# Kernel optimization log

Measured on AMD Instinct MI355X. Metric: run time of the kernel, lower is better.

The kernel has to match this reference:

```python
import jax, jax.numpy as jnp
import numpy as np

EPS = 1e-8
LN_EPS = 1e-5
TOPK = 8

B, N, D = 8, 2048, 512


def setup_inputs() -> dict:
    key = jax.random.key(0)
    ks = jax.random.split(key, 4)
    feats = jax.random.normal(ks[0], (B, N, D), dtype=jnp.float32)
    mask = jnp.ones((B, N), dtype=bool)
    # per-layer GCN weights (no bias) and LayerNorm params, plus output LN
    W1 = jax.random.normal(ks[1], (D, D), dtype=jnp.float32) / np.sqrt(D)
    W2 = jax.random.normal(ks[2], (D, D), dtype=jnp.float32) / np.sqrt(D)
    ln1_g = jnp.ones((D,), jnp.float32); ln1_b = jnp.zeros((D,), jnp.float32)
    ln2_g = jnp.ones((D,), jnp.float32); ln2_b = jnp.zeros((D,), jnp.float32)
    out_g = jnp.ones((D,), jnp.float32); out_b = jnp.zeros((D,), jnp.float32)
    return {"feats": feats, "mask": mask, "W1": W1, "ln1_g": ln1_g, "ln1_b": ln1_b,
            "W2": W2, "ln2_g": ln2_g, "ln2_b": ln2_b, "out_g": out_g, "out_b": out_b}


def _layer_norm(x, g, b):
    mu = jnp.mean(x, axis=-1, keepdims=True)
    var = jnp.mean(jnp.square(x - mu), axis=-1, keepdims=True)
    return (x - mu) * jax.lax.rsqrt(var + LN_EPS) * g + b


def build_similarity_graph(feats, mask):
    b, n, _ = feats.shape
    mask_f = mask.astype(feats.dtype)                       # [B,N]
    valid_pair = mask[:, None, :] & mask[:, :, None]        # [B,N,N]
    vp_f = valid_pair.astype(feats.dtype)
    # cosine similarity mapped to [0,1]
    fn = feats / jnp.clip(jnp.linalg.norm(feats, axis=-1, keepdims=True), EPS)
    sim = (jnp.einsum('bnd,bmd->bnm', fn, fn) + 1.0) * 0.5
    sim = sim * vp_f
    eye = jnp.eye(n, dtype=bool)
    sim_wo_self = jnp.where(eye[None], 0.0, sim)
    # top-k neighbors per node (invalid pairs pushed to -1)
    k = min(TOPK, n - 1)
    candidate = jnp.where(valid_pair, sim_wo_self, -1.0)
    values, indices = jax.lax.top_k(candidate, k)           # [B,N,k]
    bi = jnp.arange(b)[:, None, None]
    ri = jnp.arange(n)[None, :, None]
    knn_mask = jnp.zeros((b, n, n), dtype=bool).at[bi, ri, indices].set(values > 0)
    adj = sim_wo_self * knn_mask.astype(feats.dtype)
    # symmetrize, add valid self-loops, re-mask
    adj = 0.5 * (adj + jnp.swapaxes(adj, 1, 2))
    adj = adj + jnp.eye(n, dtype=feats.dtype)[None] * (mask_f[:, :, None] * mask_f[:, None, :])
    adj = adj * vp_f
    # symmetric degree normalization
    deg_inv_sqrt = jnp.clip(adj.sum(-1), EPS) ** -0.5       # [B,N]
    adj_norm = adj * deg_inv_sqrt[:, :, None] * deg_inv_sqrt[:, None, :]
    return adj_norm * vp_f


def _gcn_layer(x, adj_norm, W, g, b, mask_f):
    out = jnp.einsum('bnm,bmd->bnd', adj_norm, x @ W) + x   # residual (Identity proj)
    out = jax.nn.relu(_layer_norm(out, g, b))
    return out * mask_f[..., None]


def reference(feats, mask, W1, ln1_g, ln1_b, W2, ln2_g, ln2_b, out_g, out_b):
    mask_f = mask.astype(feats.dtype)
    x = feats * mask_f[..., None]                           # input_proj = Identity, then mask
    adj_norm = build_similarity_graph(feats, mask)
    x = _gcn_layer(x, adj_norm, W1, ln1_g, ln1_b, mask_f)
    x = _gcn_layer(x, adj_norm, W2, ln2_g, ln2_b, mask_f)
    x = _layer_norm(x, out_g, out_b)
    return x * mask_f[..., None]
```

## Files before the change

### kernel.cpp

```cpp
#include <hip/hip_runtime.h>
#include <cstdint>


constexpr int Bb   = 8;
constexpr int Nn   = 2048;
constexpr int Dd   = 512;
constexpr int BN   = Bb * Nn;
constexpr int KTOP = 8;
constexpr int CAP  = 56;
constexpr int NSLICE = 4;

typedef __attribute__((ext_vector_type(8))) __bf16 bf16x8;
typedef __attribute__((ext_vector_type(4))) __bf16 bf16x4;
typedef __attribute__((ext_vector_type(4))) float  f32x4;

__device__ __forceinline__ void gload16(const void* g, void* l) {
  __builtin_amdgcn_global_load_lds((const __attribute__((address_space(1))) unsigned int*)g,
                                   (__attribute__((address_space(3))) unsigned int*)l,
                                   16, 0, 0);
}
__device__ __forceinline__ void barrier_raw() {
  asm volatile("" ::: "memory");
  __builtin_amdgcn_s_barrier();
  asm volatile("" ::: "memory");
}

__global__ __launch_bounds__(256) void rownorm_kernel(const float* __restrict__ feats,
                                                      float* __restrict__ rinv) {
  const int row  = blockIdx.x * 4 + (threadIdx.x >> 6);
  const int lane = threadIdx.x & 63;
  const float* p = feats + (size_t)row * Dd + lane * 8;
  float4 a = *(const float4*)p;
  float4 b = *(const float4*)(p + 4);
  float s = a.x*a.x + a.y*a.y + a.z*a.z + a.w*a.w
          + b.x*b.x + b.y*b.y + b.z*b.z + b.w*b.w;
#pragma unroll
  for (int o = 32; o; o >>= 1) s += __shfl_down(s, o);
  if (lane == 0) rinv[row] = 1.0f / fmaxf(sqrtf(s), 1e-8f);
}

__global__ __launch_bounds__(256) void split_kernel(const float* __restrict__ feats,
                                                    const float* __restrict__ rinv,
                                                    __bf16* __restrict__ Hk,
                                                    __bf16* __restrict__ Lk,
                                                    __bf16* __restrict__ Xk) {
  __shared__ float tile[64][65];
  __shared__ float rsh[64];
  const int r0 = blockIdx.x * 64;
  const int bz = r0 >> 11;
  const int n0 = r0 & 2047;
  const int t  = threadIdx.x;
  if (t < 64) rsh[t] = rinv[r0 + t];

  for (int kt = 0; kt < 8; ++kt) {
    __syncthreads();
#pragma unroll
    for (int p = 0; p < 4; ++p) {
      const int row = p * 16 + (t >> 4), ch = t & 15;
      float4 v = *(const float4*)(feats + (size_t)(r0 + row) * Dd + kt * 64 + ch * 4);
      tile[row][ch * 4 + 0] = v.x; tile[row][ch * 4 + 1] = v.y;
      tile[row][ch * 4 + 2] = v.z; tile[row][ch * 4 + 3] = v.w;
    }
    __syncthreads();
#pragma unroll
    for (int h = 0; h < 2; ++h) {
      const int c = h * 256 + t;
      const int k8l = c >> 6, row = c & 63;
      const float s = rsh[row];
      bf16x8 hv, lv, xv;
#pragma unroll
      for (int e = 0; e < 8; ++e) {
        const float x = tile[row][k8l * 8 + e];
        xv[e] = (__bf16)x;
        const float nm = x * s;
        const __bf16 hh = (__bf16)nm;
        hv[e] = hh;
        lv[e] = (__bf16)(nm - (float)hh);
      }
      const size_t kk = (size_t)(kt * 8 + k8l);
      *(bf16x8*)(Hk + ((size_t)(bz * 64) + kk) * (Nn * 8) + (n0 + row) * 8) = hv;
      *(bf16x8*)(Lk + ((size_t)(bz * 64) + kk) * (Nn * 8) + (n0 + row) * 8) = lv;
      *(bf16x8*)(Xk + kk * ((size_t)BN * 8) + (size_t)(r0 + row) * 8) = xv;
    }
  }
}

__global__ __launch_bounds__(256) void wcast_t(const float* __restrict__ W,
                                               __bf16* __restrict__ Wk) {
  __shared__ float t[32][33];
  const int bx = blockIdx.x * 32, by = blockIdx.y * 32;
  const int lx = threadIdx.x & 31, ly = threadIdx.x >> 5;
#pragma unroll
  for (int r = 0; r < 32; r += 8)
    t[ly + r][lx] = W[(size_t)(by + ly + r) * Dd + bx + lx];
  __syncthreads();
  if (threadIdx.x < 128) {
    const int k8l = threadIdx.x >> 5, nl = threadIdx.x & 31;
    bf16x8 v;
#pragma unroll
    for (int e = 0; e < 8; ++e) v[e] = (__bf16)t[k8l * 8 + e][nl];
    *(bf16x8*)(Wk + ((size_t)((by >> 3) + k8l) * Dd + bx + nl) * 8) = v;
  }
}

__device__ __forceinline__ void ins8(float (&tv)[8], int (&ti)[8], float v, int idx) {
#pragma unroll
  for (int q = 0; q < 8; ++q) {
    bool sw = v > tv[q];
    float a = sw ? tv[q] : v;
    int   c = sw ? ti[q] : idx;
    tv[q] = sw ? v   : tv[q];
    ti[q] = sw ? idx : ti[q];
    v = a; idx = c;
  }
}
__device__ __forceinline__ void ins8t(float (&tv)[8], int (&ti)[8], float v, int idx) {
#pragma unroll
  for (int q = 0; q < 8; ++q) {
    bool sw = (v > tv[q]) || (v == tv[q] && idx < ti[q]);
    float a = sw ? tv[q] : v;
    int   c = sw ? ti[q] : idx;
    tv[q] = sw ? v   : tv[q];
    ti[q] = sw ? idx : ti[q];
    v = a; idx = c;
  }
}

__global__ __launch_bounds__(256, 2) void sim_mfma_topk(const __bf16* __restrict__ Hk,
                                                        const __bf16* __restrict__ Lk,
                                                        float* __restrict__ pv,
                                                        int* __restrict__ pi) {
  __shared__ __align__(16) char smem[65536];

  const int f     = blockIdx.x;
  const int bz    = f & 7;
  const int rr    = f >> 3;
  const int r0    = (rr & 15) * 128;
  const int slice = rr >> 4;

  const int tid    = threadIdx.x;
  const int lane   = tid & 63;
  const int lane15 = tid & 15;
  const int kgrp   = (tid >> 4) & 3;
  const int wv     = tid >> 6;
  const int wrow0  = wv * 32;
  const int bN     = bz * Nn;

  const __bf16* Hb = Hk + (size_t)(bz * 64) * (Nn * 8);
  const __bf16* Lb = Lk + (size_t)(bz * 64) * (Nn * 8);

  float t8v[2][8]; int t8i[2][8];
#pragma unroll
  for (int rs = 0; rs < 2; ++rs)
#pragma unroll
    for (int q = 0; q < 8; ++q) { t8v[rs][q] = -1.0f; t8i[rs][q] = 0; }

  auto stage = [&](int t, int buf) {
    const int ct = t >> 4, k80 = (t & 15) << 2;
    const int rbase = (wv < 2) ? r0 : slice * 512 + ct * 128;
    const __bf16* base = ((wv & 1) == 0) ? Hb : Lb;
    char* ldsb = smem + buf * 32768 + wv * 8192;
#pragma unroll
    for (int i = 0; i < 8; ++i) {
      const int kg = i >> 1, rb = (i & 1) << 6;
      gload16(base + ((size_t)(k80 + kg) * Nn + rbase + rb + lane) * 8,
              ldsb + kg * 2048 + rb * 16);
    }
  };

  f32x4 acc[2][8];
  const f32x4 z = {0.f, 0.f, 0.f, 0.f};

  stage(0, 0);
  for (int t = 0; t < 64; ++t) {
    const int cur = t & 1;
    if ((t & 15) == 0) {
#pragma unroll
      for (int i = 0; i < 2; ++i)
#pragma unroll
        for (int j = 0; j < 8; ++j) acc[i][j] = z;
    }
    if (t + 1 < 64) {
      stage(t + 1, cur ^ 1);
      asm volatile("s_waitcnt vmcnt(8)" ::: "memory");
    } else {
      asm volatile("s_waitcnt vmcnt(0)" ::: "memory");
    }
    barrier_raw();

    const char* sb = smem + cur * 32768;
    const int a0o = kgrp * 2048 + (wrow0 + lane15) * 16;
    bf16x8 ah0 = *(const bf16x8*)(sb + a0o);
    bf16x8 ah1 = *(const bf16x8*)(sb + a0o + 256);
    bf16x8 al0 = *(const bf16x8*)(sb + 8192 + a0o);
    bf16x8 al1 = *(const bf16x8*)(sb + 8192 + a0o + 256);
#pragma unroll
    for (int cs = 0; cs < 8; ++cs) {
      const int bo = kgrp * 2048 + (cs * 16 + lane15) * 16;
      bf16x8 bh = *(const bf16x8*)(sb + 16384 + bo);
      bf16x8 bl = *(const bf16x8*)(sb + 24576 + bo);
      acc[0][cs] = __builtin_amdgcn_mfma_f32_16x16x32_bf16(bh, ah0, acc[0][cs], 0, 0, 0);
      acc[0][cs] = __builtin_amdgcn_mfma_f32_16x16x32_bf16(bl, ah0, acc[0][cs], 0, 0, 0);
      acc[0][cs] = __builtin_amdgcn_mfma_f32_16x16x32_bf16(bh, al0, acc[0][cs], 0, 0, 0);
      acc[1][cs] = __builtin_amdgcn_mfma_f32_16x16x32_bf16(bh, ah1, acc[1][cs], 0, 0, 0);
      acc[1][cs] = __builtin_amdgcn_mfma_f32_16x16x32_bf16(bl, ah1, acc[1][cs], 0, 0, 0);
      acc[1][cs] = __builtin_amdgcn_mfma_f32_16x16x32_bf16(bh, al1, acc[1][cs], 0, 0, 0);
    }
    barrier_raw();

    if ((t & 15) == 15) {
      const int ct = t >> 4;
      const int ctile0 = slice * 512 + ct * 128;
#pragma unroll
      for (int rs = 0; rs < 2; ++rs) {
        const int rowg = r0 + wrow0 + rs * 16 + lane15;
#pragma unroll
        for (int cs = 0; cs < 8; ++cs)
#pragma unroll
          for (int e = 0; e < 4; ++e) {
            const int col = ctile0 + cs * 16 + kgrp * 4 + e;
            const float v = (acc[rs][cs][e] + 1.0f) * 0.5f;
            if (col != rowg && v > t8v[rs][7]) ins8(t8v[rs], t8i[rs], v, col);
          }
      }
    }
  }

#pragma unroll
  for (int rs = 0; rs < 2; ++rs) {
#pragma unroll
    for (int m = 16; m <= 32; m <<= 1) {
      float ov[8]; int oi[8];
#pragma unroll
      for (int q = 0; q < 8; ++q) {
        ov[q] = __shfl_xor(t8v[rs][q], m);
        oi[q] = __shfl_xor(t8i[rs][q], m);
      }
#pragma unroll
      for (int q = 0; q < 8; ++q)
        if (ov[q] > t8v[rs][7] || (ov[q] == t8v[rs][7] && oi[q] < t8i[rs][7]))
          ins8t(t8v[rs], t8i[rs], ov[q], oi[q]);
    }
  }

  if (lane < 16) {
#pragma unroll
    for (int rs = 0; rs < 2; ++rs) {
      const int prow = bN + r0 + wrow0 + rs * 16 + lane15;
#pragma unroll
      for (int q = 0; q < 8; ++q) {
        pv[(prow * NSLICE + slice) * 8 + q] = t8v[rs][q];
        pi[(prow * NSLICE + slice) * 8 + q] = bN + t8i[rs][q];
      }
    }
  }
}

__global__ __launch_bounds__(256) void merge_edges(const float* __restrict__ pv,
                                                   const int* __restrict__ pi,
                                                   int* __restrict__ ecnt,
                                                   int* __restrict__ eidx,
                                                   float* __restrict__ ew) {
  const int row = blockIdx.x * 256 + threadIdx.x;
  if (row >= BN) return;
  float tv[8]; int ti[8];
#pragma unroll
  for (int q = 0; q < 8; ++q) { tv[q] = -1.0f; ti[q] = 0; }
  for (int s = 0; s < NSLICE; ++s)
#pragma unroll
    for (int q = 0; q < 8; ++q) {
      const float v = pv[(row * NSLICE + s) * 8 + q];
      if (v > tv[7]) ins8(tv, ti, v, pi[(row * NSLICE + s) * 8 + q]);
    }
#pragma unroll
  for (int t = 0; t < KTOP; ++t) {
    if (tv[t] > 0.0f) {
      const int j = ti[t];
      const float w = 0.5f * tv[t];
      int p = atomicAdd(&ecnt[row], 1);
      if (p < CAP) { eidx[row * CAP + p] = j; ew[row * CAP + p] = w; }
      int q2 = atomicAdd(&ecnt[j], 1);
      if (q2 < CAP) { eidx[j * CAP + q2] = row; ew[j * CAP + q2] = w; }
    }
  }
}

__global__ __launch_bounds__(256) void deg_kernel(const int* __restrict__ ecnt,
                                                  const float* __restrict__ ew,
                                                  float* __restrict__ dis) {
  const int r = blockIdx.x * 256 + threadIdx.x;
  if (r >= BN) return;
  const int cnt = min(ecnt[r], CAP);
  float d = 1.0f;
  for (int e = 0; e < cnt; ++e) d += ew[r * CAP + e];
  dis[r] = rsqrtf(fmaxf(d, 1e-8f));
}

__global__ __launch_bounds__(256, 2) void gemm_mfma(const __bf16* __restrict__ Xk,
                                                    const __bf16* __restrict__ Wk,
                                                    __bf16* __restrict__ Yb) {
  __shared__ __align__(16) char smem[32768];
  const int tid    = threadIdx.x;
  const int lane   = tid & 63;
  const int lane15 = tid & 15;
  const int kgrp   = (tid >> 4) & 3;
  const int wv     = tid >> 6;
  const int m0 = blockIdx.x * 128, n0 = blockIdx.y * 128;

  auto stage = [&](int t, int buf) {
    const int k80 = t << 2;
#pragma unroll
    for (int i = 0; i < 4; ++i) {
      const int c = (wv << 2) + i;
      const int kg = (c & 7) >> 1, rb = (c & 1) << 6;
      const __bf16* g = (c >> 3)
          ? Wk + ((size_t)(k80 + kg) * Dd + n0 + rb + lane) * 8
          : Xk + ((size_t)(k80 + kg) * BN + m0 + rb + lane) * 8;
      gload16(g, smem + buf * 16384 + ((c >> 3) << 13) + kg * 2048 + rb * 16);
    }
  };

  f32x4 acc[2][8];
  const f32x4 z = {0.f, 0.f, 0.f, 0.f};
#pragma unroll
  for (int i = 0; i < 2; ++i)
#pragma unroll
    for (int j = 0; j < 8; ++j) acc[i][j] = z;

  stage(0, 0);
  for (int t = 0; t < 16; ++t) {
    const int cur = t & 1;
    if (t + 1 < 16) {
      stage(t + 1, cur ^ 1);
      asm volatile("s_waitcnt vmcnt(4)" ::: "memory");
    } else {
      asm volatile("s_waitcnt vmcnt(0)" ::: "memory");
    }
    barrier_raw();

    const char* sb = smem + cur * 16384;
    const int a0o = kgrp * 2048 + (wv * 32 + lane15) * 16;
    bf16x8 a0 = *(const bf16x8*)(sb + a0o);
    bf16x8 a1 = *(const bf16x8*)(sb + a0o + 256);
#pragma unroll
    for (int cs = 0; cs < 8; ++cs) {
      bf16x8 b = *(const bf16x8*)(sb + 8192 + kgrp * 2048 + (cs * 16 + lane15) * 16);
      acc[0][cs] = __builtin_amdgcn_mfma_f32_16x16x32_bf16(b, a0, acc[0][cs], 0, 0, 0);
      acc[1][cs] = __builtin_amdgcn_mfma_f32_16x16x32_bf16(b, a1, acc[1][cs], 0, 0, 0);
    }
    barrier_raw();
  }
#pragma unroll
  for (int rs = 0; rs < 2; ++rs) {
    const int row = m0 + wv * 32 + rs * 16 + lane15;
#pragma unroll
    for (int cs = 0; cs < 8; ++cs) {
      bf16x4 o;
#pragma unroll
      for (int e = 0; e < 4; ++e) o[e] = (__bf16)acc[rs][cs][e];
      *(bf16x4*)(Yb + (size_t)row * Dd + n0 + cs * 16 + kgrp * 4) = o;
    }
  }
}

__device__ __forceinline__ void breduce2_128(float& s, float& q, float* red) {
#pragma unroll
  for (int o = 32; o; o >>= 1) { s += __shfl_down(s, o); q += __shfl_down(q, o); }
  __syncthreads();
  if ((threadIdx.x & 63) == 0) {
    red[(threadIdx.x >> 6) * 2]     = s;
    red[(threadIdx.x >> 6) * 2 + 1] = q;
  }
  __syncthreads();
  s = red[0] + red[2];
  q = red[1] + red[3];
}

template <bool FINAL>
__global__ __launch_bounds__(128) void agg_ln_kernel(const __bf16* __restrict__ yb,
                                                     const float* __restrict__ xres_f,
                                                     const __bf16* __restrict__ xres_k,
                                                     const int* __restrict__ ecnt,
                                                     const int* __restrict__ eidx,
                                                     const float* __restrict__ ew,
                                                     const float* __restrict__ dis,
                                                     const float* __restrict__ g1,
                                                     const float* __restrict__ b1v,
                                                     const float* __restrict__ g2,
                                                     const float* __restrict__ b2v,
                                                     float* __restrict__ outf,
                                                     __bf16* __restrict__ outk) {
  __shared__ float red[4];
  const int row = (blockIdx.x & 7) * Nn + (blockIdx.x >> 3);
  const int tid = threadIdx.x;
  const int d0 = tid * 4;
  const float di = dis[row];

  bf16x4 yv = *(const bf16x4*)(yb + (size_t)row * Dd + d0);
  float a[4];
#pragma unroll
  for (int e2 = 0; e2 < 4; ++e2) a[e2] = di * di * (float)yv[e2];
  const int cnt = min(ecnt[row], CAP);
  for (int e = 0; e < cnt; ++e) {
    const int j = eidx[row * CAP + e];
    const float c = ew[row * CAP + e] * di * dis[j];
    bf16x4 v = *(const bf16x4*)(yb + (size_t)j * Dd + d0);
#pragma unroll
    for (int e2 = 0; e2 < 4; ++e2) a[e2] += c * (float)v[e2];
  }
  if (FINAL) {
    bf16x4 u = *(const bf16x4*)(xres_k + ((size_t)(tid >> 1) * BN + row) * 8 + (tid & 1) * 4);
#pragma unroll
    for (int e2 = 0; e2 < 4; ++e2) a[e2] += (float)u[e2];
  } else {
    float4 xv = *(const float4*)(xres_f + (size_t)row * Dd + d0);
    a[0] += xv.x; a[1] += xv.y; a[2] += xv.z; a[3] += xv.w;
  }

  float s = a[0] + a[1] + a[2] + a[3];
  float qq = a[0]*a[0] + a[1]*a[1] + a[2]*a[2] + a[3]*a[3];
  breduce2_128(s, qq, red);
  const float mu = s * (1.0f / Dd);
  const float var = qq * (1.0f / Dd) - mu * mu;
  const float rs = rsqrtf(var + 1e-5f);
  float4 g = *(const float4*)(g1 + d0);
  float4 bb = *(const float4*)(b1v + d0);
  float tv[4];
  tv[0] = fmaxf((a[0] - mu) * rs * g.x + bb.x, 0.0f);
  tv[1] = fmaxf((a[1] - mu) * rs * g.y + bb.y, 0.0f);
  tv[2] = fmaxf((a[2] - mu) * rs * g.z + bb.z, 0.0f);
  tv[3] = fmaxf((a[3] - mu) * rs * g.w + bb.w, 0.0f);

  if (FINAL) {
    float s2 = tv[0] + tv[1] + tv[2] + tv[3];
    float q2 = tv[0]*tv[0] + tv[1]*tv[1] + tv[2]*tv[2] + tv[3]*tv[3];
    breduce2_128(s2, q2, red);
    const float mu2 = s2 * (1.0f / Dd);
    const float var2 = q2 * (1.0f / Dd) - mu2 * mu2;
    const float rs2 = rsqrtf(var2 + 1e-5f);
    float4 g2v = *(const float4*)(g2 + d0);
    float4 b2 = *(const float4*)(b2v + d0);
    float4 o;
    o.x = (tv[0] - mu2) * rs2 * g2v.x + b2.x;
    o.y = (tv[1] - mu2) * rs2 * g2v.y + b2.y;
    o.z = (tv[2] - mu2) * rs2 * g2v.z + b2.z;
    o.w = (tv[3] - mu2) * rs2 * g2v.w + b2.w;
    *(float4*)(outf + (size_t)row * Dd + d0) = o;
  } else {
    bf16x4 ov;
#pragma unroll
    for (int e2 = 0; e2 < 4; ++e2) ov[e2] = (__bf16)tv[e2];
    *(bf16x4*)(outk + ((size_t)(tid >> 1) * BN + row) * 8 + (tid & 1) * 4) = ov;
  }
}

extern "C" void kernel_launch(void* const* d_in, const int* in_sizes, int n_in,
                              void* d_out, int out_size, void* d_ws, size_t ws_size,
                              hipStream_t stream) {
  const float* feats = (const float*)d_in[0];
  const float* W1    = (const float*)d_in[2];
  const float* ln1_g = (const float*)d_in[3];
  const float* ln1_b = (const float*)d_in[4];
  const float* W2    = (const float*)d_in[5];
  const float* ln2_g = (const float*)d_in[6];
  const float* ln2_b = (const float*)d_in[7];
  const float* out_g = (const float*)d_in[8];
  const float* out_b = (const float*)d_in[9];
  float* out = (float*)d_out;

  char* w = (char*)d_ws;
  float* rinv = (float*)w; w += (size_t)BN * 4;
  float* topv = (float*)w; w += (size_t)BN * KTOP * 4;
  int*   topi = (int*)w;   w += (size_t)BN * KTOP * 4;
  int*   ecnt = (int*)w;   w += (size_t)BN * 4;
  int*   eidx = (int*)w;   w += (size_t)BN * CAP * 4;
  float* ew   = (float*)w; w += (size_t)BN * CAP * 4;
  float* dis  = (float*)w; w += (size_t)BN * 4;
  __bf16* Wk1 = (__bf16*)w; w += (size_t)Dd * Dd * 2;
  __bf16* Wk2 = (__bf16*)w; w += (size_t)Dd * Dd * 2;
  float* ybuf = (float*)w; w += (size_t)BN * Dd * 4;
  __bf16* Xk  = (__bf16*)w; w += (size_t)BN * Dd * 2;
  __bf16* h1k = (__bf16*)w; w += (size_t)BN * Dd * 2;
  __bf16* Hk = (__bf16*)ybuf;
  __bf16* Lk = Hk + (size_t)BN * Dd;
  __bf16* Yb = (__bf16*)ybuf;
  float* pv  = (float*)h1k;
  int*   pi  = (int*)((char*)h1k + (size_t)BN * NSLICE * 8 * 4);
  (void)topv; (void)topi;

  hipMemsetAsync(ecnt, 0, (size_t)BN * 4, stream);

  rownorm_kernel<<<BN / 4, 256, 0, stream>>>(feats, rinv);
  split_kernel<<<BN / 64, 256, 0, stream>>>(feats, rinv, Hk, Lk, Xk);
  wcast_t<<<dim3(16, 16), 256, 0, stream>>>(W1, Wk1);
  wcast_t<<<dim3(16, 16), 256, 0, stream>>>(W2, Wk2);

  sim_mfma_topk<<<512, 256, 0, stream>>>(Hk, Lk, pv, pi);
  merge_edges<<<BN / 256, 256, 0, stream>>>(pv, pi, ecnt, eidx, ew);
  deg_kernel<<<BN / 256, 256, 0, stream>>>(ecnt, ew, dis);

  gemm_mfma<<<dim3(BN / 128, Dd / 128), 256, 0, stream>>>(Xk, Wk1, Yb);
  agg_ln_kernel<false><<<BN, 128, 0, stream>>>(Yb, feats, nullptr, ecnt, eidx, ew, dis,
                                               ln1_g, ln1_b, nullptr, nullptr,
                                               nullptr, h1k);
  gemm_mfma<<<dim3(BN / 128, Dd / 128), 256, 0, stream>>>(h1k, Wk2, Yb);
  agg_ln_kernel<true><<<BN, 128, 0, stream>>>(Yb, nullptr, h1k, ecnt, eidx, ew, dis,
                                              ln2_g, ln2_b, out_g, out_b,
                                              out, nullptr);
}
```

Baseline: 315.2 us.

## Replace split-bf16 similarity with single bf16 pass plus fp32 top-k refinement

The similarity GEMM drops the hi/lo bf16 split (three MFMAs per tile) and uses a single bf16 product, halving LDS staging and allowing more slices and blocks. Each slice keeps its approximate top-8. A new refine kernel picks the 12 best candidates per row from the 64 and recomputes their exact fp32 cosine from feats before choosing the final top-8. The row-norm kernel is folded into split_kernel. In exchange, a true neighbour that bf16 rounding pushes out of a slice's top-8 or outside the 12 refined candidates would be missed.

```diff
diff --git a/kernel.cpp b/kernel.cpp
--- a/kernel.cpp
+++ b/kernel.cpp
@@ -8,7 +8,7 @@
 constexpr int BN   = Bb * Nn;
 constexpr int KTOP = 8;
 constexpr int CAP  = 56;
-constexpr int NSLICE = 4;
+constexpr int NSLICE = 8;
 
 typedef __attribute__((ext_vector_type(8))) __bf16 bf16x8;
 typedef __attribute__((ext_vector_type(4))) __bf16 bf16x4;
@@ -25,24 +25,9 @@
   asm volatile("" ::: "memory");
 }
 
-__global__ __launch_bounds__(256) void rownorm_kernel(const float* __restrict__ feats,
-                                                      float* __restrict__ rinv) {
-  const int row  = blockIdx.x * 4 + (threadIdx.x >> 6);
-  const int lane = threadIdx.x & 63;
-  const float* p = feats + (size_t)row * Dd + lane * 8;
-  float4 a = *(const float4*)p;
-  float4 b = *(const float4*)(p + 4);
-  float s = a.x*a.x + a.y*a.y + a.z*a.z + a.w*a.w
-          + b.x*b.x + b.y*b.y + b.z*b.z + b.w*b.w;
-#pragma unroll
-  for (int o = 32; o; o >>= 1) s += __shfl_down(s, o);
-  if (lane == 0) rinv[row] = 1.0f / fmaxf(sqrtf(s), 1e-8f);
-}
-
 __global__ __launch_bounds__(256) void split_kernel(const float* __restrict__ feats,
-                                                    const float* __restrict__ rinv,
+                                                    float* __restrict__ rinv,
                                                     __bf16* __restrict__ Hk,
-                                                    __bf16* __restrict__ Lk,
                                                     __bf16* __restrict__ Xk) {
   __shared__ float tile[64][65];
   __shared__ float rsh[64];
@@ -50,7 +35,23 @@
   const int bz = r0 >> 11;
   const int n0 = r0 & 2047;
   const int t  = threadIdx.x;
-  if (t < 64) rsh[t] = rinv[r0 + t];
+  const int wv = t >> 6, lane = t & 63;
+
+  for (int i = 0; i < 16; ++i) {
+    const int row = wv * 16 + i;
+    const float* p = feats + (size_t)(r0 + row) * Dd + lane * 8;
+    float4 a = *(const float4*)p;
+    float4 b = *(const float4*)(p + 4);
+    float s = a.x*a.x + a.y*a.y + a.z*a.z + a.w*a.w
+            + b.x*b.x + b.y*b.y + b.z*b.z + b.w*b.w;
+#pragma unroll
+    for (int o = 32; o; o >>= 1) s += __shfl_down(s, o);
+    if (lane == 0) {
+      const float ri = 1.0f / fmaxf(sqrtf(s), 1e-8f);
+      rsh[row] = ri;
+      rinv[r0 + row] = ri;
+    }
+  }
 
   for (int kt = 0; kt < 8; ++kt) {
     __syncthreads();
@@ -67,19 +68,15 @@
       const int c = h * 256 + t;
       const int k8l = c >> 6, row = c & 63;
       const float s = rsh[row];
-      bf16x8 hv, lv, xv;
+      bf16x8 hv, xv;
 #pragma unroll
       for (int e = 0; e < 8; ++e) {
         const float x = tile[row][k8l * 8 + e];
         xv[e] = (__bf16)x;
-        const float nm = x * s;
-        const __bf16 hh = (__bf16)nm;
-        hv[e] = hh;
-        lv[e] = (__bf16)(nm - (float)hh);
+        hv[e] = (__bf16)(x * s);
       }
       const size_t kk = (size_t)(kt * 8 + k8l);
       *(bf16x8*)(Hk + ((size_t)(bz * 64) + kk) * (Nn * 8) + (n0 + row) * 8) = hv;
-      *(bf16x8*)(Lk + ((size_t)(bz * 64) + kk) * (Nn * 8) + (n0 + row) * 8) = lv;
       *(bf16x8*)(Xk + kk * ((size_t)BN * 8) + (size_t)(r0 + row) * 8) = xv;
     }
   }
@@ -126,11 +123,10 @@
   }
 }
 
-__global__ __launch_bounds__(256, 2) void sim_mfma_topk(const __bf16* __restrict__ Hk,
-                                                        const __bf16* __restrict__ Lk,
-                                                        float* __restrict__ pv,
-                                                        int* __restrict__ pi) {
-  __shared__ __align__(16) char smem[65536];
+__global__ __launch_bounds__(256, 3) void sim_hh_topk(const __bf16* __restrict__ Hk,
+                                                      float* __restrict__ pv,
+                                                      int* __restrict__ pi) {
+  __shared__ __align__(16) char smem[32768];
 
   const int f     = blockIdx.x;
   const int bz    = f & 7;
@@ -147,7 +143,6 @@
   const int bN     = bz * Nn;
 
   const __bf16* Hb = Hk + (size_t)(bz * 64) * (Nn * 8);
-  const __bf16* Lb = Lk + (size_t)(bz * 64) * (Nn * 8);
 
   float t8v[2][8]; int t8i[2][8];
 #pragma unroll
@@ -157,14 +152,16 @@
 
   auto stage = [&](int t, int buf) {
     const int ct = t >> 4, k80 = (t & 15) << 2;
-    const int rbase = (wv < 2) ? r0 : slice * 512 + ct * 128;
-    const __bf16* base = ((wv & 1) == 0) ? Hb : Lb;
-    char* ldsb = smem + buf * 32768 + wv * 8192;
-#pragma unroll
-    for (int i = 0; i < 8; ++i) {
-      const int kg = i >> 1, rb = (i & 1) << 6;
-      gload16(base + ((size_t)(k80 + kg) * Nn + rbase + rb + lane) * 8,
-              ldsb + kg * 2048 + rb * 16);
+    const int c0 = slice * 256 + ct * 128;
+#pragma unroll
+    for (int i = 0; i < 4; ++i) {
+      const int c = (wv << 2) + i;
+      const bool isB = c >= 8;
+      const int cc = isB ? c - 8 : c;
+      const int kg = cc >> 1, rb = cc & 1;
+      const int rbase = (isB ? c0 : r0) + rb * 64 + lane;
+      gload16(Hb + ((size_t)(k80 + kg) * Nn + rbase) * 8,
+              smem + buf * 16384 + (isB ? 8192 : 0) + kg * 2048 + (rb * 64 + lane) * 16);
     }
   };
 
@@ -172,7 +169,7 @@
   const f32x4 z = {0.f, 0.f, 0.f, 0.f};
 
   stage(0, 0);
-  for (int t = 0; t < 64; ++t) {
+  for (int t = 0; t < 32; ++t) {
     const int cur = t & 1;
     if ((t & 15) == 0) {
 #pragma unroll
@@ -180,37 +177,29 @@
 #pragma unroll
         for (int j = 0; j < 8; ++j) acc[i][j] = z;
     }
-    if (t + 1 < 64) {
+    if (t + 1 < 32) {
       stage(t + 1, cur ^ 1);
-      asm volatile("s_waitcnt vmcnt(8)" ::: "memory");
+      asm volatile("s_waitcnt vmcnt(4)" ::: "memory");
     } else {
       asm volatile("s_waitcnt vmcnt(0)" ::: "memory");
     }
     barrier_raw();
 
-    const char* sb = smem + cur * 32768;
+    const char* sb = smem + cur * 16384;
     const int a0o = kgrp * 2048 + (wrow0 + lane15) * 16;
     bf16x8 ah0 = *(const bf16x8*)(sb + a0o);
     bf16x8 ah1 = *(const bf16x8*)(sb + a0o + 256);
-    bf16x8 al0 = *(const bf16x8*)(sb + 8192 + a0o);
-    bf16x8 al1 = *(const bf16x8*)(sb + 8192 + a0o + 256);
 #pragma unroll
     for (int cs = 0; cs < 8; ++cs) {
-      const int bo = kgrp * 2048 + (cs * 16 + lane15) * 16;
-      bf16x8 bh = *(const bf16x8*)(sb + 16384 + bo);
-      bf16x8 bl = *(const bf16x8*)(sb + 24576 + bo);
+      bf16x8 bh = *(const bf16x8*)(sb + 8192 + kgrp * 2048 + (cs * 16 + lane15) * 16);
       acc[0][cs] = __builtin_amdgcn_mfma_f32_16x16x32_bf16(bh, ah0, acc[0][cs], 0, 0, 0);
-      acc[0][cs] = __builtin_amdgcn_mfma_f32_16x16x32_bf16(bl, ah0, acc[0][cs], 0, 0, 0);
-      acc[0][cs] = __builtin_amdgcn_mfma_f32_16x16x32_bf16(bh, al0, acc[0][cs], 0, 0, 0);
       acc[1][cs] = __builtin_amdgcn_mfma_f32_16x16x32_bf16(bh, ah1, acc[1][cs], 0, 0, 0);
-      acc[1][cs] = __builtin_amdgcn_mfma_f32_16x16x32_bf16(bl, ah1, acc[1][cs], 0, 0, 0);
-      acc[1][cs] = __builtin_amdgcn_mfma_f32_16x16x32_bf16(bh, al1, acc[1][cs], 0, 0, 0);
     }
     barrier_raw();
 
     if ((t & 15) == 15) {
       const int ct = t >> 4;
-      const int ctile0 = slice * 512 + ct * 128;
+      const int ctile0 = slice * 256 + ct * 128;
 #pragma unroll
       for (int rs = 0; rs < 2; ++rs) {
         const int rowg = r0 + wrow0 + rs * 16 + lane15;
@@ -249,38 +238,78 @@
       const int prow = bN + r0 + wrow0 + rs * 16 + lane15;
 #pragma unroll
       for (int q = 0; q < 8; ++q) {
-        pv[(prow * NSLICE + slice) * 8 + q] = t8v[rs][q];
-        pi[(prow * NSLICE + slice) * 8 + q] = bN + t8i[rs][q];
+        pv[((size_t)prow * NSLICE + slice) * 8 + q] = t8v[rs][q];
+        pi[((size_t)prow * NSLICE + slice) * 8 + q] = bN + t8i[rs][q];
       }
     }
   }
 }
 
-__global__ __launch_bounds__(256) void merge_edges(const float* __restrict__ pv,
-                                                   const int* __restrict__ pi,
-                                                   int* __restrict__ ecnt,
-                                                   int* __restrict__ eidx,
-                                                   float* __restrict__ ew) {
-  const int row = blockIdx.x * 256 + threadIdx.x;
-  if (row >= BN) return;
-  float tv[8]; int ti[8];
-#pragma unroll
-  for (int q = 0; q < 8; ++q) { tv[q] = -1.0f; ti[q] = 0; }
-  for (int s = 0; s < NSLICE; ++s)
-#pragma unroll
-    for (int q = 0; q < 8; ++q) {
-      const float v = pv[(row * NSLICE + s) * 8 + q];
-      if (v > tv[7]) ins8(tv, ti, v, pi[(row * NSLICE + s) * 8 + q]);
-    }
-#pragma unroll
-  for (int t = 0; t < KTOP; ++t) {
-    if (tv[t] > 0.0f) {
-      const int j = ti[t];
-      const float w = 0.5f * tv[t];
-      int p = atomicAdd(&ecnt[row], 1);
-      if (p < CAP) { eidx[row * CAP + p] = j; ew[row * CAP + p] = w; }
-      int q2 = atomicAdd(&ecnt[j], 1);
-      if (q2 < CAP) { eidx[j * CAP + q2] = row; ew[j * CAP + q2] = w; }
+__global__ __launch_bounds__(256) void refine_edges(const float* __restrict__ feats,
+                                                    const float* __restrict__ rinv,
+                                                    const float* __restrict__ pv,
+                                                    const int* __restrict__ pi,
+                                                    int* __restrict__ ecnt,
+                                                    int* __restrict__ eidx,
+                                                    float* __restrict__ ew) {
+  const int f  = blockIdx.x;
+  const int bz = f & 7;
+  const int wv = threadIdx.x >> 6;
+  const int lane = threadIdx.x & 63;
+  const int row = bz * Nn + (f >> 3) * 4 + wv;
+
+  float scr = pv[(size_t)row * 64 + lane];
+  int   sid = pi[(size_t)row * 64 + lane];
+
+  const float* xi = feats + (size_t)row * Dd + lane * 8;
+  const float4 xi0 = *(const float4*)xi;
+  const float4 xi1 = *(const float4*)(xi + 4);
+  const float  ri  = rinv[row];
+
+  int ridx[12];
+#pragma unroll
+  for (int c = 0; c < 12; ++c) {
+    float mv = scr; int mi = sid;
+#pragma unroll
+    for (int o = 32; o; o >>= 1) {
+      const float ov = __shfl_xor(mv, o);
+      const int   oi = __shfl_xor(mi, o);
+      if (ov > mv || (ov == mv && oi < mi)) { mv = ov; mi = oi; }
+    }
+    if (sid == mi) scr = -2.0f;
+    ridx[c] = mi;
+  }
+
+  float rv[12];
+#pragma unroll
+  for (int c = 0; c < 12; ++c) {
+    const float* xc = feats + (size_t)ridx[c] * Dd + lane * 8;
+    const float4 c0 = *(const float4*)xc;
+    const float4 c1 = *(const float4*)(xc + 4);
+    float d = xi0.x*c0.x + xi0.y*c0.y + xi0.z*c0.z + xi0.w*c0.w
+            + xi1.x*c1.x + xi1.y*c1.y + xi1.z*c1.z + xi1.w*c1.w;
+#pragma unroll
+    for (int o = 32; o; o >>= 1) d += __shfl_xor(d, o);
+    rv[c] = (d * ri * rinv[ridx[c]] + 1.0f) * 0.5f;
+  }
+
+  float t8v[8]; int t8i[8];
+#pragma unroll
+  for (int q = 0; q < 8; ++q) { t8v[q] = -1.0f; t8i[q] = 0x7fffffff; }
+#pragma unroll
+  for (int c = 0; c < 12; ++c) ins8t(t8v, t8i, rv[c], ridx[c]);
+
+  if (lane == 0) {
+#pragma unroll
+    for (int q = 0; q < KTOP; ++q) {
+      if (t8v[q] > 0.0f) {
+        const int j = t8i[q];
+        const float w = 0.5f * t8v[q];
+        int p = atomicAdd(&ecnt[row], 1);
+        if (p < CAP) { eidx[row * CAP + p] = j; ew[row * CAP + p] = w; }
+        int q2 = atomicAdd(&ecnt[j], 1);
+        if (q2 < CAP) { eidx[j * CAP + q2] = row; ew[j * CAP + q2] = w; }
+      }
     }
   }
 }
@@ -470,8 +499,6 @@
 
   char* w = (char*)d_ws;
   float* rinv = (float*)w; w += (size_t)BN * 4;
-  float* topv = (float*)w; w += (size_t)BN * KTOP * 4;
-  int*   topi = (int*)w;   w += (size_t)BN * KTOP * 4;
   int*   ecnt = (int*)w;   w += (size_t)BN * 4;
   int*   eidx = (int*)w;   w += (size_t)BN * CAP * 4;
   float* ew   = (float*)w; w += (size_t)BN * CAP * 4;
@@ -482,21 +509,18 @@
   __bf16* Xk  = (__bf16*)w; w += (size_t)BN * Dd * 2;
   __bf16* h1k = (__bf16*)w; w += (size_t)BN * Dd * 2;
   __bf16* Hk = (__bf16*)ybuf;
-  __bf16* Lk = Hk + (size_t)BN * Dd;
   __bf16* Yb = (__bf16*)ybuf;
   float* pv  = (float*)h1k;
   int*   pi  = (int*)((char*)h1k + (size_t)BN * NSLICE * 8 * 4);
-  (void)topv; (void)topi;
 
   hipMemsetAsync(ecnt, 0, (size_t)BN * 4, stream);
 
-  rownorm_kernel<<<BN / 4, 256, 0, stream>>>(feats, rinv);
-  split_kernel<<<BN / 64, 256, 0, stream>>>(feats, rinv, Hk, Lk, Xk);
+  split_kernel<<<BN / 64, 256, 0, stream>>>(feats, rinv, Hk, Xk);
   wcast_t<<<dim3(16, 16), 256, 0, stream>>>(W1, Wk1);
   wcast_t<<<dim3(16, 16), 256, 0, stream>>>(W2, Wk2);
 
-  sim_mfma_topk<<<512, 256, 0, stream>>>(Hk, Lk, pv, pi);
-  merge_edges<<<BN / 256, 256, 0, stream>>>(pv, pi, ecnt, eidx, ew);
+  sim_hh_topk<<<1024, 256, 0, stream>>>(Hk, pv, pi);
+  refine_edges<<<BN / 4, 256, 0, stream>>>(feats, rinv, pv, pi, ecnt, eidx, ew);
   deg_kernel<<<BN / 256, 256, 0, stream>>>(ecnt, ew, dis);
 
   gemm_mfma<<<dim3(BN / 128, Dd / 128), 256, 0, stream>>>(Xk, Wk1, Yb);
```

New measurement: 333.8 us. 5.9% more time.
